# Optimization experiments

Hardware: AMD Instinct MI355X
Metric: run time of the kernel (lower is better)

Reference implementation:

```python
import jax, jax.numpy as jnp
import numpy as np

NUM_HEADS = 16
NEG_INF = -1e18


def setup_inputs() -> dict:
    key = jax.random.key(0)
    ks = jax.random.split(key, 9)
    T, B, D = 2048, 2, 1024
    s = 1.0 / np.sqrt(D)
    return {
        "query": jax.random.normal(ks[0], (T, B, D), jnp.float32),
        "q_w": jax.random.normal(ks[1], (D, D), jnp.float32) * s,
        "q_b": jax.random.normal(ks[2], (D,), jnp.float32) * 0.02,
        "k_w": jax.random.normal(ks[3], (D, D), jnp.float32) * s,
        "k_b": jax.random.normal(ks[4], (D,), jnp.float32) * 0.02,
        "v_w": jax.random.normal(ks[5], (D, D), jnp.float32) * s,
        "v_b": jax.random.normal(ks[6], (D,), jnp.float32) * 0.02,
        "out_w": jax.random.normal(ks[7], (D, D), jnp.float32) * s,
        "out_b": jax.random.normal(ks[8], (D,), jnp.float32) * 0.02,
    }


def reference(query, q_w, q_b, k_w, k_b, v_w, v_b, out_w, out_b):
    # query: [T, B, D] (Time x Batch x Channel). Self-attention, causal mask,
    # dropout=0, need_weights=True.
    T, B, D = query.shape
    H = NUM_HEADS
    hd = D // H
    scaling = 1.0 / jnp.sqrt(jnp.asarray(hd, query.dtype))

    q = (query @ q_w.T + q_b) * scaling
    k = query @ k_w.T + k_b
    v = query @ v_w.T + v_b

    def split_heads(x):  # [T, B, D] -> [B, H, T, hd]
        return x.reshape(T, B, H, hd).transpose(1, 2, 0, 3)

    qh, kh, vh = split_heads(q), split_heads(k), split_heads(v)

    # scores: [B, H, T, T]
    scores = jnp.einsum("bhtd,bhsd->bhts", qh, kh)
    causal = jnp.triu(jnp.full((T, T), NEG_INF, dtype=scores.dtype), k=1)
    scores = scores + causal

    probs = jax.nn.softmax(scores, axis=-1)
    attn = jnp.einsum("bhts,bhsd->bhtd", probs, vh)  # [B, H, T, hd]
    attn = attn.transpose(2, 0, 1, 3).reshape(T, B, D)
    out = attn @ out_w.T + out_b

    # averaged attention weights over heads: [B, T, T]
    avg_weights = probs.sum(axis=1) / H
    return out, avg_weights
```

## Files before the change

kernel.cpp:

```cpp
#include <hip/hip_runtime.h>
#include <hip/hip_bf16.h>
#include <stdint.h>

typedef __hip_bfloat16 bf16;
using short8 = __attribute__((ext_vector_type(8))) short;
using f32x4  = __attribute__((ext_vector_type(4))) float;

#define TDIM 2048
#define BDIM 2
#define DDIM 1024
#define HNUM 16
#define HD   64
#define MDIM 4096
#define M0   16.0f
#define L2E  1.44269504088896f
#define M0B  23.0831207f

__device__ __forceinline__ f32x4 mfma16(short8 a, short8 b, f32x4 c) {
  return __builtin_amdgcn_mfma_f32_16x16x32_bf16(a, b, c, 0, 0, 0);
}

__device__ __forceinline__ float fexp2(float s) {
  return __builtin_amdgcn_exp2f(__builtin_fmaf(s, L2E, -M0B));
}

#define GLD16(G, L)                                              \
  __builtin_amdgcn_global_load_lds(                              \
      (const __attribute__((address_space(1))) void*)(G),        \
      (__attribute__((address_space(3))) void*)(L), 16, 0, 0)

union S8 { short8 v; bf16 h[8]; };
union P4 { uint2 u; bf16 h[4]; };

__global__ __launch_bounds__(256) void cast_all_kernel(
    const float* __restrict__ q, const float* __restrict__ wq,
    const float* __restrict__ wk, const float* __restrict__ wv,
    const float* __restrict__ wo, bf16* __restrict__ dst) {
  int t4 = blockIdx.x * blockDim.x + threadIdx.x;
  int idx = t4 * 4;
  const float* s;
  if (idx < 4194304)      s = q  + idx;
  else if (idx < 5242880) s = wq + (idx - 4194304);
  else if (idx < 6291456) s = wk + (idx - 5242880);
  else if (idx < 7340032) s = wv + (idx - 6291456);
  else                    s = wo + (idx - 7340032);
  float4 v = *(const float4*)s;
  union { ushort4 u; bf16 b[4]; } pk;
  pk.b[0] = __float2bfloat16(v.x);
  pk.b[1] = __float2bfloat16(v.y);
  pk.b[2] = __float2bfloat16(v.z);
  pk.b[3] = __float2bfloat16(v.w);
  *(ushort4*)(dst + idx) = pk.u;
}

__global__ __launch_bounds__(256, 2) void qkv_kernel(
    const bf16* __restrict__ X, const bf16* __restrict__ Wq,
    const bf16* __restrict__ Wk, const bf16* __restrict__ Wv,
    const float* __restrict__ qb, const float* __restrict__ kb,
    const float* __restrict__ vb, bf16* __restrict__ Qo,
    bf16* __restrict__ Ko, bf16* __restrict__ Vto) {
  __shared__ __align__(16) bf16 Xs[128][72];
  __shared__ __align__(16) bf16 Qs[64][72];
  __shared__ __align__(16) bf16 Ks[64][72];
  __shared__ __align__(16) bf16 Vs[64][72];
  const int tid  = threadIdx.x;
  const int lane = tid & 63, wave = tid >> 6;
  const int m0 = blockIdx.y * 128, n0 = blockIdx.x * 64;
  const int wm = (wave >> 1) * 64, wn = (wave & 1) * 32;
  const int fr = lane & 15, quad = lane >> 4, q8 = quad * 8;
  const int r = tid >> 3, cc = (tid & 7) * 8;
  f32x4 aq[4][2] = {}, ak[4][2] = {}, av[2][4] = {};
  const bf16* xp = X  + (size_t)(m0 + r) * DDIM + cc;
  const bf16* qp = Wq + (size_t)(n0 + r) * DDIM + cc;
  const bf16* kp = Wk + (size_t)(n0 + r) * DDIM + cc;
  const bf16* vp = Wv + (size_t)(n0 + r) * DDIM + cc;
  uint4 xv0, xv1, xv2, xv3, qv0, qv1, kv0, kv1, vv0, vv1;
#define QKV_LD(K0)                                                  \
  do {                                                              \
    xv0 = *(const uint4*)(xp + (K0));                               \
    xv1 = *(const uint4*)(xp + (size_t)32 * DDIM + (K0));           \
    xv2 = *(const uint4*)(xp + (size_t)64 * DDIM + (K0));           \
    xv3 = *(const uint4*)(xp + (size_t)96 * DDIM + (K0));           \
    qv0 = *(const uint4*)(qp + (K0));                               \
    qv1 = *(const uint4*)(qp + (size_t)32 * DDIM + (K0));           \
    kv0 = *(const uint4*)(kp + (K0));                               \
    kv1 = *(const uint4*)(kp + (size_t)32 * DDIM + (K0));           \
    vv0 = *(const uint4*)(vp + (K0));                               \
    vv1 = *(const uint4*)(vp + (size_t)32 * DDIM + (K0));           \
  } while (0)
  QKV_LD(0);
  for (int k0 = 0; k0 < DDIM; k0 += 64) {
    __syncthreads();
    *(uint4*)&Xs[r][cc]      = xv0;
    *(uint4*)&Xs[r + 32][cc] = xv1;
    *(uint4*)&Xs[r + 64][cc] = xv2;
    *(uint4*)&Xs[r + 96][cc] = xv3;
    *(uint4*)&Qs[r][cc]      = qv0;
    *(uint4*)&Qs[r + 32][cc] = qv1;
    *(uint4*)&Ks[r][cc]      = kv0;
    *(uint4*)&Ks[r + 32][cc] = kv1;
    *(uint4*)&Vs[r][cc]      = vv0;
    *(uint4*)&Vs[r + 32][cc] = vv1;
    __syncthreads();
    if (k0 + 64 < DDIM) QKV_LD(k0 + 64);
#pragma unroll
    for (int kk = 0; kk < 2; kk++) {
      const int ko = kk * 32 + q8;
      short8 xf[4], qf[2], kf[2], vf[2];
#pragma unroll
      for (int i = 0; i < 4; i++)
        xf[i] = *(const short8*)&Xs[wm + i * 16 + fr][ko];
#pragma unroll
      for (int j = 0; j < 2; j++) {
        qf[j] = *(const short8*)&Qs[wn + j * 16 + fr][ko];
        kf[j] = *(const short8*)&Ks[wn + j * 16 + fr][ko];
        vf[j] = *(const short8*)&Vs[wn + j * 16 + fr][ko];
      }
#pragma unroll
      for (int i = 0; i < 4; i++)
#pragma unroll
        for (int j = 0; j < 2; j++) {
          aq[i][j] = mfma16(xf[i], qf[j], aq[i][j]);
          ak[i][j] = mfma16(xf[i], kf[j], ak[i][j]);
          av[j][i] = mfma16(vf[j], xf[i], av[j][i]);
        }
    }
  }
#undef QKV_LD
#pragma unroll
  for (int mt = 0; mt < 4; mt++)
#pragma unroll
    for (int nt = 0; nt < 2; nt++)
#pragma unroll
      for (int i = 0; i < 4; i++) {
        int gm = m0 + wm + mt * 16 + quad * 4 + i;
        int gn = n0 + wn + nt * 16 + fr;
        int t = gm >> 1, bb = gm & 1, h = gn >> 6, e = gn & 63;
        size_t o = ((size_t)(bb * HNUM + h) * TDIM + t) * HD + e;
        Qo[o] = __float2bfloat16((aq[mt][nt][i] + qb[gn]) * 0.125f);
        Ko[o] = __float2bfloat16(ak[mt][nt][i] + kb[gn]);
      }
#pragma unroll
  for (int vt = 0; vt < 2; vt++)
#pragma unroll
    for (int xt = 0; xt < 4; xt++)
#pragma unroll
      for (int i = 0; i < 4; i++) {
        int gf = n0 + wn + vt * 16 + quad * 4 + i;
        int gt = m0 + wm + xt * 16 + fr;
        int t = gt >> 1, bb = gt & 1, h = gf >> 6, e = gf & 63;
        Vto[((size_t)(bb * HNUM + h) * HD + e) * TDIM + t] =
            __float2bfloat16(av[vt][xt][i] + vb[gf]);
      }
}

__global__ __launch_bounds__(256) void combine_kernel(
    const bf16* __restrict__ P0, const bf16* __restrict__ P1,
    const float* __restrict__ l0buf, const float* __restrict__ l1buf,
    bf16* __restrict__ A) {
  const int idx = (blockIdx.x * 256 + threadIdx.x) * 8;
  const int m = idx >> 10, col = idx & 1023;
  const int t = m >> 1, bb = m & 1, h = col >> 6;
  const size_t li = (size_t)(bb * HNUM + h) * TDIM + t;
  const float inv = 1.0f / (l0buf[li] + l1buf[li]);
  S8 a0, a1, w;
  a0.v = *(const short8*)&P0[idx];
  a1.v = *(const short8*)&P1[idx];
#pragma unroll
  for (int k = 0; k < 8; k++)
    w.h[k] = __float2bfloat16(
        (__bfloat162float(a0.h[k]) + __bfloat162float(a1.h[k])) * inv);
  *(short8*)&A[idx] = w.v;
}

__global__ __launch_bounds__(256) void gemm_out_kernel(
    const bf16* __restrict__ A, const bf16* __restrict__ Bw,
    const float* __restrict__ bias, float* __restrict__ of32) {
  __shared__ __align__(16) bf16 As[64][72];
  __shared__ __align__(16) bf16 Bs[64][72];
  const int tid  = threadIdx.x;
  const int lane = tid & 63, wave = tid >> 6;
  const int m0 = blockIdx.y * 64, n0 = blockIdx.x * 64;
  const int wm = (wave >> 1) * 32, wn = (wave & 1) * 32;
  const int fr = lane & 15, quad = lane >> 4, q8 = quad * 8;
  const int ldr = tid >> 3, ldc = (tid & 7) * 8;
  f32x4 acc[2][2] = {};
  const bf16* ap0 = A + (size_t)(m0 + ldr) * DDIM + ldc;
  const bf16* ap1 = ap0 + (size_t)32 * DDIM;
  const bf16* bp0 = Bw + (size_t)(n0 + ldr) * DDIM + ldc;
  const bf16* bp1 = bp0 + (size_t)32 * DDIM;
  uint4 av0, av1, bv0, bv1;
#define OUT_LD(K0)                                  \
  do {                                              \
    av0 = *(const uint4*)(ap0 + (K0));              \
    av1 = *(const uint4*)(ap1 + (K0));              \
    bv0 = *(const uint4*)(bp0 + (K0));              \
    bv1 = *(const uint4*)(bp1 + (K0));              \
  } while (0)
  OUT_LD(0);
  for (int k0 = 0; k0 < DDIM; k0 += 64) {
    __syncthreads();
    *(uint4*)&As[ldr][ldc]      = av0;
    *(uint4*)&As[ldr + 32][ldc] = av1;
    *(uint4*)&Bs[ldr][ldc]      = bv0;
    *(uint4*)&Bs[ldr + 32][ldc] = bv1;
    __syncthreads();
    if (k0 + 64 < DDIM) OUT_LD(k0 + 64);
#pragma unroll
    for (int kk = 0; kk < 2; kk++) {
      const int ko = kk * 32 + q8;
      short8 af0, af1, bf0, bf1;
      af0 = *(const short8*)&As[wm + fr][ko];
      af1 = *(const short8*)&As[wm + 16 + fr][ko];
      bf0 = *(const short8*)&Bs[wn + fr][ko];
      bf1 = *(const short8*)&Bs[wn + 16 + fr][ko];
      acc[0][0] = mfma16(af0, bf0, acc[0][0]);
      acc[0][1] = mfma16(af0, bf1, acc[0][1]);
      acc[1][0] = mfma16(af1, bf0, acc[1][0]);
      acc[1][1] = mfma16(af1, bf1, acc[1][1]);
    }
  }
#undef OUT_LD
#pragma unroll
  for (int mt = 0; mt < 2; mt++)
#pragma unroll
    for (int nt = 0; nt < 2; nt++)
#pragma unroll
      for (int i = 0; i < 4; i++) {
        int gm = m0 + wm + mt * 16 + quad * 4 + i;
        int gn = n0 + wn + nt * 16 + fr;
        of32[(size_t)gm * DDIM + gn] = acc[mt][nt][i] + bias[gn];
      }
}

__global__ __launch_bounds__(256) void attn_split_kernel(
    const bf16* __restrict__ Q, const bf16* __restrict__ K,
    const bf16* __restrict__ Vt, bf16* __restrict__ P0o,
    bf16* __restrict__ P1o, float* __restrict__ l0buf,
    float* __restrict__ l1buf) {
  __shared__ __align__(16) bf16 Ks[2][64][40];
  __shared__ __align__(16) bf16 Vs[2][64][40];
  __shared__ __align__(16) bf16 pt[4][32][72];
  const int tid = threadIdx.x, lane = tid & 63, wave = tid >> 6;
  const int bid = blockIdx.x;
  const int part = bid & 1, bh = (bid >> 1) & 31, t128 = 15 - (bid >> 6);
  const int b = bh >> 4, h = bh & 15;
  const int t0 = t128 * 128 + wave * 32;
  const int fr = lane & 15, quad = lane >> 4, q8 = quad * 8;
  const bf16* Qp = Q + ((size_t)bh * TDIM + t0) * HD;
  const bf16* Kp = K + (size_t)bh * TDIM * HD;
  const bf16* Vp = Vt + (size_t)bh * HD * TDIM;
  short8 aq[2][2];
  aq[0][0] = *(const short8*)&Qp[fr * HD + q8];
  aq[0][1] = *(const short8*)&Qp[fr * HD + 32 + q8];
  aq[1][0] = *(const short8*)&Qp[(16 + fr) * HD + q8];
  aq[1][1] = *(const short8*)&Qp[(16 + fr) * HD + 32 + q8];
  const int Cb = 2 * t128 + 2, C0 = t128 + 1;
  const int clo = part ? C0 : 0, chi = part ? Cb : C0;
  const int sr0 = tid >> 3, scc = (tid & 7) * 8, sr1 = sr0 + 32;
  const int ssub = scc >> 5, scol = scc & 31;
  f32x4 oacc[2][4] = {};
  float lsum[2] = {0.f, 0.f};
  uint4 kv0, kv1, vv0, vv1;
  auto ldglob = [&](int c) {
    int s0 = c * 64;
    kv0 = *(const uint4*)&Kp[(size_t)(s0 + sr0) * HD + scc];
    kv1 = *(const uint4*)&Kp[(size_t)(s0 + sr1) * HD + scc];
    vv0 = *(const uint4*)&Vp[(size_t)sr0 * TDIM + s0 + scc];
    vv1 = *(const uint4*)&Vp[(size_t)sr1 * TDIM + s0 + scc];
  };
  ldglob(clo);
  for (int c = clo; c < chi; c++) {
    __syncthreads();
    *(uint4*)&Ks[ssub][sr0][scol] = kv0;
    *(uint4*)&Ks[ssub][sr1][scol] = kv1;
    *(uint4*)&Vs[ssub][sr0][scol] = vv0;
    *(uint4*)&Vs[ssub][sr1][scol] = vv1;
    __syncthreads();
    if (c + 1 < chi) ldglob(c + 1);
    const int s0 = c * 64;
    if (s0 > t0 + 31) continue;
    f32x4 scT[2][4] = {};
#pragma unroll
    for (int j = 0; j < 4; j++) {
      short8 k0f = *(const short8*)&Ks[0][j * 16 + fr][q8];
      short8 k1f = *(const short8*)&Ks[1][j * 16 + fr][q8];
      scT[0][j] = mfma16(k0f, aq[0][0], scT[0][j]);
      scT[0][j] = mfma16(k1f, aq[0][1], scT[0][j]);
      scT[1][j] = mfma16(k0f, aq[1][0], scT[1][j]);
      scT[1][j] = mfma16(k1f, aq[1][1], scT[1][j]);
    }
#pragma unroll
    for (int g = 0; g < 2; g++) {
      const int tg = t0 + g * 16;
#pragma unroll
      for (int j = 0; j < 4; j++) {
        const int sj = s0 + j * 16;
        P4 pk;
        if (sj > tg + 15) {
          pk.u = make_uint2(0u, 0u);
        } else if (sj + 15 <= tg) {
#pragma unroll
          for (int i = 0; i < 4; i++) {
            float p = fexp2(scT[g][j][i]);
            lsum[g] += p;
            pk.h[i] = __float2bfloat16(p);
          }
        } else {
          const int t_row = tg + fr;
          const int s_base = sj + quad * 4;
#pragma unroll
          for (int i = 0; i < 4; i++) {
            float p = 0.f;
            if (s_base + i <= t_row) {
              p = fexp2(scT[g][j][i]);
              lsum[g] += p;
            }
            pk.h[i] = __float2bfloat16(p);
          }
        }
        *(uint2*)&pt[wave][g * 16 + fr][j * 16 + quad * 4] = pk.u;
      }
    }
#pragma unroll
    for (int c2 = 0; c2 < 2; c2++) {
      short8 ap0 = *(const short8*)&pt[wave][fr][c2 * 32 + q8];
      short8 ap1 = *(const short8*)&pt[wave][16 + fr][c2 * 32 + q8];
#pragma unroll
      for (int nt = 0; nt < 4; nt++) {
        short8 vf = *(const short8*)&Vs[c2][nt * 16 + fr][q8];
        oacc[0][nt] = mfma16(ap0, vf, oacc[0][nt]);
        oacc[1][nt] = mfma16(ap1, vf, oacc[1][nt]);
      }
    }
  }
  float lr[2];
#pragma unroll
  for (int g = 0; g < 2; g++) {
    float l = lsum[g];
    l += __shfl_xor(l, 16);
    l += __shfl_xor(l, 32);
    lr[g] = l;
  }
  bf16*  Op = part ? P1o : P0o;
  float* lb = part ? l1buf : l0buf;
#pragma unroll
  for (int g = 0; g < 2; g++)
#pragma unroll
    for (int nt = 0; nt < 4; nt++)
#pragma unroll
      for (int i = 0; i < 4; i++) {
        int t_row = t0 + g * 16 + quad * 4 + i;
        int col = h * HD + nt * 16 + fr;
        Op[((size_t)t_row * BDIM + b) * DDIM + col] =
            __float2bfloat16(oacc[g][nt][i]);
      }
  if (quad == 0) {
    lb[(size_t)bh * TDIM + t0 + fr]      = lr[0];
    lb[(size_t)bh * TDIM + t0 + 16 + fr] = lr[1];
  }
}

__global__ __launch_bounds__(256) void avg_kernel(
    const bf16* __restrict__ Q, const bf16* __restrict__ K,
    const float* __restrict__ l0buf, const float* __restrict__ l1buf,
    float* __restrict__ avgw) {
  const int tid = threadIdx.x;
  int r = blockIdx.x;
  const int b = (r >= 2048) ? 1 : 0;
  r &= 2047;
  float* avp = avgw + (size_t)b * TDIM * TDIM;
  if (r >= 1056) {
    int r2 = r - 1056;
    int ti = 0;
    while (ti < 31 && (ti + 1) * (62 - ti) <= r2) ti++;
    int si = (2 * ti + 2) + (r2 - ti * (63 - ti));
    int t0b = ti * 64, s0 = si * 32;
#pragma unroll
    for (int k = 0; k < 2; k++) {
      int off = (tid * 2 + k) * 4;
      *(float4*)&avp[(size_t)(t0b + (off >> 5)) * TDIM + s0 + (off & 31)] =
          make_float4(0.f, 0.f, 0.f, 0.f);
    }
    return;
  }
  int ti = 0;
  while ((ti + 1) * (ti + 2) <= r) ti++;
  const int si = r - ti * (ti + 1);
  const int t0b = ti * 64, s0 = si * 32;

  __shared__ __align__(16) bf16 Qs[2][64][64];
  __shared__ __align__(16) bf16 Ks2[2][32][64];
  __shared__ float sinvl[HNUM][64];
#pragma unroll
  for (int k = 0; k < 4; k++) {
    int idx = tid + k * 256;
    size_t li = (size_t)(b * HNUM + (idx >> 6)) * TDIM + t0b + (idx & 63);
    sinvl[idx >> 6][idx & 63] = 1.0f / (l0buf[li] + l1buf[li]);
  }
  const int lane = tid & 63, wave = tid >> 6;
  const int fr = lane & 15, quad = lane >> 4;
  const int twr = wave * 16, tw = t0b + twr;
  const int srow8 = lane >> 3;
  const int scol = (((lane & 7) ^ (srow8 & 7))) * 8;
  const bf16* Qb = Q + (size_t)b * HNUM * TDIM * HD;
  const bf16* Kb = K + (size_t)b * HNUM * TDIM * HD;
#define AVG_STAGE(B, HH)                                                      \
  do {                                                                        \
    const bf16* Qh_ = Qb + (size_t)(HH) * TDIM * HD;                          \
    const bf16* Kh_ = Kb + (size_t)(HH) * TDIM * HD;                          \
    GLD16(Qh_ + (size_t)(t0b + 16 * wave + srow8) * HD + scol,                \
          &Qs[B][16 * wave][0]);                                              \
    GLD16(Qh_ + (size_t)(t0b + 16 * wave + 8 + srow8) * HD + scol,            \
          &Qs[B][16 * wave + 8][0]);                                          \
    GLD16(Kh_ + (size_t)(s0 + 8 * wave + srow8) * HD + scol,                  \
          &Ks2[B][8 * wave][0]);                                              \
  } while (0)
  AVG_STAGE(0, 0);
  const int sA0 = ((quad)     ^ (fr & 7)) * 8;
  const int sA1 = ((4 + quad) ^ (fr & 7)) * 8;
  f32x4 facc[2] = {};
  const bool d0 = (s0 > tw + 15),      f0 = (s0 + 15 <= tw);
  const bool d1 = (s0 + 16 > tw + 15), f1 = (s0 + 31 <= tw);
  for (int hh = 0; hh < HNUM; hh++) {
    const int cur = hh & 1;
    __syncthreads();
    if (hh + 1 < HNUM) AVG_STAGE(cur ^ 1, hh + 1);
    f32x4 sv = *(const f32x4*)&sinvl[hh][twr + quad * 4];
    short8 a0 = *(const short8*)&Qs[cur][twr + fr][sA0];
    short8 a1 = *(const short8*)&Qs[cur][twr + fr][sA1];
    if (!d0) {
      short8 b0 = *(const short8*)&Ks2[cur][fr][sA0];
      short8 b1 = *(const short8*)&Ks2[cur][fr][sA1];
      f32x4 sc = {};
      sc = mfma16(a0, b0, sc);
      sc = mfma16(a1, b1, sc);
      if (f0) {
#pragma unroll
        for (int i = 0; i < 4; i++)
          facc[0][i] += fexp2(sc[i]) * sv[i];
      } else {
#pragma unroll
        for (int i = 0; i < 4; i++)
          if (s0 + fr <= tw + quad * 4 + i)
            facc[0][i] += fexp2(sc[i]) * sv[i];
      }
    }
    if (!d1) {
      short8 b0 = *(const short8*)&Ks2[cur][16 + fr][sA0];
      short8 b1 = *(const short8*)&Ks2[cur][16 + fr][sA1];
      f32x4 sc = {};
      sc = mfma16(a0, b0, sc);
      sc = mfma16(a1, b1, sc);
      if (f1) {
#pragma unroll
        for (int i = 0; i < 4; i++)
          facc[1][i] += fexp2(sc[i]) * sv[i];
      } else {
#pragma unroll
        for (int i = 0; i < 4; i++)
          if (s0 + 16 + fr <= tw + quad * 4 + i)
            facc[1][i] += fexp2(sc[i]) * sv[i];
      }
    }
  }
#undef AVG_STAGE
#pragma unroll
  for (int nt = 0; nt < 2; nt++)
#pragma unroll
    for (int i = 0; i < 4; i++)
      avp[(size_t)(t0b + twr + quad * 4 + i) * TDIM + s0 + nt * 16 + fr] =
          facc[nt][i] * 0.0625f;
}

extern "C" void kernel_launch(void* const* d_in, const int* in_sizes, int n_in,
                              void* d_out, int out_size, void* d_ws, size_t ws_size,
                              hipStream_t stream) {
  const float* q   = (const float*)d_in[0];
  const float* q_w = (const float*)d_in[1];
  const float* q_b = (const float*)d_in[2];
  const float* k_w = (const float*)d_in[3];
  const float* k_b = (const float*)d_in[4];
  const float* v_w = (const float*)d_in[5];
  const float* v_b = (const float*)d_in[6];
  const float* o_w = (const float*)d_in[7];
  const float* o_b = (const float*)d_in[8];
  float* out = (float*)d_out;
  float* avg = out + (size_t)MDIM * DDIM;

  bf16* ws  = (bf16*)d_ws;
  bf16* Xbf = ws;
  bf16* Wq  = ws + 4194304;
  bf16* Wk  = ws + 5242880;
  bf16* Wv  = ws + 6291456;
  bf16* Wo  = ws + 7340032;
  bf16* Qw  = ws + 8388608;
  bf16* Kw  = ws + 12582912;
  bf16* Vt  = ws + 16777216;
  bf16* P1  = ws + 20971520;
  bf16* P0  = ws;
  bf16* Ab  = ws + 16777216;
  float* l0 = (float*)(ws + 4194304);
  float* l1 = (float*)(ws + 4325376);

  cast_all_kernel<<<8192, 256, 0, stream>>>(q, q_w, k_w, v_w, o_w, Xbf);
  qkv_kernel<<<dim3(16, 32), 256, 0, stream>>>(Xbf, Wq, Wk, Wv, q_b, k_b, v_b,
                                               Qw, Kw, Vt);
  attn_split_kernel<<<1024, 256, 0, stream>>>(Qw, Kw, Vt, P0, P1, l0, l1);
  combine_kernel<<<2048, 256, 0, stream>>>(P0, P1, l0, l1, Ab);
  avg_kernel<<<4096, 256, 0, stream>>>(Qw, Kw, l0, l1, avg);
  gemm_out_kernel<<<dim3(16, 64), 256, 0, stream>>>(Ab, Wo, o_b, out);
}
```

Before: 222.1 us.

## Enlarge output GEMM and head-averaged weight tiles for more reuse

The output projection GEMM now computes 128x64 tiles per block, with each wave owning a 64x32 sub-tile, which halves the grid and reuses B-fragments across more MFMAs. The avg_kernel now processes 64x64 causal score tiles instead of 64x32, so each Q tile staged per head serves twice as many keys. Its block indexing is reworked for the new triangular enumeration, while the zero-fill blocks stay in 32-column units. Larger tiles mean more registers and LDS per block and fewer blocks, which may reduce occupancy and load balance.

Result: slower. 228.0 us (+2.6%).

```diff
diff --git a/kernel.cpp b/kernel.cpp
--- a/kernel.cpp
+++ b/kernel.cpp
@@ -173,56 +173,61 @@
   *(short8*)&A[idx] = w.v;
 }
 
-__global__ __launch_bounds__(256) void gemm_out_kernel(
+__global__ __launch_bounds__(256, 2) void gemm_out_kernel(
     const bf16* __restrict__ A, const bf16* __restrict__ Bw,
     const float* __restrict__ bias, float* __restrict__ of32) {
-  __shared__ __align__(16) bf16 As[64][72];
+  __shared__ __align__(16) bf16 As[128][72];
   __shared__ __align__(16) bf16 Bs[64][72];
   const int tid  = threadIdx.x;
   const int lane = tid & 63, wave = tid >> 6;
-  const int m0 = blockIdx.y * 64, n0 = blockIdx.x * 64;
-  const int wm = (wave >> 1) * 32, wn = (wave & 1) * 32;
+  const int m0 = blockIdx.y * 128, n0 = blockIdx.x * 64;
+  const int wm = (wave >> 1) * 64, wn = (wave & 1) * 32;
   const int fr = lane & 15, quad = lane >> 4, q8 = quad * 8;
-  const int ldr = tid >> 3, ldc = (tid & 7) * 8;
-  f32x4 acc[2][2] = {};
-  const bf16* ap0 = A + (size_t)(m0 + ldr) * DDIM + ldc;
-  const bf16* ap1 = ap0 + (size_t)32 * DDIM;
-  const bf16* bp0 = Bw + (size_t)(n0 + ldr) * DDIM + ldc;
-  const bf16* bp1 = bp0 + (size_t)32 * DDIM;
-  uint4 av0, av1, bv0, bv1;
-#define OUT_LD(K0)                                  \
-  do {                                              \
-    av0 = *(const uint4*)(ap0 + (K0));              \
-    av1 = *(const uint4*)(ap1 + (K0));              \
-    bv0 = *(const uint4*)(bp0 + (K0));              \
-    bv1 = *(const uint4*)(bp1 + (K0));              \
+  const int r = tid >> 3, cc = (tid & 7) * 8;
+  f32x4 acc[4][2] = {};
+  const bf16* ap = A  + (size_t)(m0 + r) * DDIM + cc;
+  const bf16* bp = Bw + (size_t)(n0 + r) * DDIM + cc;
+  uint4 av0, av1, av2, av3, bv0, bv1;
+#define OUT_LD(K0)                                                  \
+  do {                                                              \
+    av0 = *(const uint4*)(ap + (K0));                               \
+    av1 = *(const uint4*)(ap + (size_t)32 * DDIM + (K0));           \
+    av2 = *(const uint4*)(ap + (size_t)64 * DDIM + (K0));           \
+    av3 = *(const uint4*)(ap + (size_t)96 * DDIM + (K0));           \
+    bv0 = *(const uint4*)(bp + (K0));                               \
+    bv1 = *(const uint4*)(bp + (size_t)32 * DDIM + (K0));           \
   } while (0)
   OUT_LD(0);
   for (int k0 = 0; k0 < DDIM; k0 += 64) {
     __syncthreads();
-    *(uint4*)&As[ldr][ldc]      = av0;
-    *(uint4*)&As[ldr + 32][ldc] = av1;
-    *(uint4*)&Bs[ldr][ldc]      = bv0;
-    *(uint4*)&Bs[ldr + 32][ldc] = bv1;
+    *(uint4*)&As[r][cc]      = av0;
+    *(uint4*)&As[r + 32][cc] = av1;
+    *(uint4*)&As[r + 64][cc] = av2;
+    *(uint4*)&As[r + 96][cc] = av3;
+    *(uint4*)&Bs[r][cc]      = bv0;
+    *(uint4*)&Bs[r + 32][cc] = bv1;
     __syncthreads();
     if (k0 + 64 < DDIM) OUT_LD(k0 + 64);
 #pragma unroll
     for (int kk = 0; kk < 2; kk++) {
       const int ko = kk * 32 + q8;
-      short8 af0, af1, bf0, bf1;
-      af0 = *(const short8*)&As[wm + fr][ko];
-      af1 = *(const short8*)&As[wm + 16 + fr][ko];
-      bf0 = *(const short8*)&Bs[wn + fr][ko];
-      bf1 = *(const short8*)&Bs[wn + 16 + fr][ko];
-      acc[0][0] = mfma16(af0, bf0, acc[0][0]);
-      acc[0][1] = mfma16(af0, bf1, acc[0][1]);
-      acc[1][0] = mfma16(af1, bf0, acc[1][0]);
-      acc[1][1] = mfma16(af1, bf1, acc[1][1]);
+      short8 af[4], bfr[2];
+#pragma unroll
+      for (int i = 0; i < 4; i++)
+        af[i] = *(const short8*)&As[wm + i * 16 + fr][ko];
+#pragma unroll
+      for (int j = 0; j < 2; j++)
+        bfr[j] = *(const short8*)&Bs[wn + j * 16 + fr][ko];
+#pragma unroll
+      for (int i = 0; i < 4; i++)
+#pragma unroll
+        for (int j = 0; j < 2; j++)
+          acc[i][j] = mfma16(af[i], bfr[j], acc[i][j]);
     }
   }
 #undef OUT_LD
 #pragma unroll
-  for (int mt = 0; mt < 2; mt++)
+  for (int mt = 0; mt < 4; mt++)
 #pragma unroll
     for (int nt = 0; nt < 2; nt++)
 #pragma unroll
@@ -367,11 +372,11 @@
     float* __restrict__ avgw) {
   const int tid = threadIdx.x;
   int r = blockIdx.x;
-  const int b = (r >= 2048) ? 1 : 0;
-  r &= 2047;
+  const int b = (r >= 1520) ? 1 : 0;
+  if (b) r -= 1520;
   float* avp = avgw + (size_t)b * TDIM * TDIM;
-  if (r >= 1056) {
-    int r2 = r - 1056;
+  if (r >= 528) {
+    int r2 = r - 528;
     int ti = 0;
     while (ti < 31 && (ti + 1) * (62 - ti) <= r2) ti++;
     int si = (2 * ti + 2) + (r2 - ti * (63 - ti));
@@ -385,12 +390,12 @@
     return;
   }
   int ti = 0;
-  while ((ti + 1) * (ti + 2) <= r) ti++;
-  const int si = r - ti * (ti + 1);
-  const int t0b = ti * 64, s0 = si * 32;
+  while ((ti + 1) * (ti + 2) / 2 <= r) ti++;
+  const int kp = r - ti * (ti + 1) / 2;
+  const int t0b = ti * 64, sA = kp * 64;
 
   __shared__ __align__(16) bf16 Qs[2][64][64];
-  __shared__ __align__(16) bf16 Ks2[2][32][64];
+  __shared__ __align__(16) bf16 Ks[2][64][64];
   __shared__ float sinvl[HNUM][64];
 #pragma unroll
   for (int k = 0; k < 4; k++) {
@@ -402,7 +407,7 @@
   const int fr = lane & 15, quad = lane >> 4;
   const int twr = wave * 16, tw = t0b + twr;
   const int srow8 = lane >> 3;
-  const int scol = (((lane & 7) ^ (srow8 & 7))) * 8;
+  const int scol = ((lane & 7) ^ (srow8 & 7)) * 8;
   const bf16* Qb = Q + (size_t)b * HNUM * TDIM * HD;
   const bf16* Kb = K + (size_t)b * HNUM * TDIM * HD;
 #define AVG_STAGE(B, HH)                                                      \
@@ -413,64 +418,60 @@
           &Qs[B][16 * wave][0]);                                              \
     GLD16(Qh_ + (size_t)(t0b + 16 * wave + 8 + srow8) * HD + scol,            \
           &Qs[B][16 * wave + 8][0]);                                          \
-    GLD16(Kh_ + (size_t)(s0 + 8 * wave + srow8) * HD + scol,                  \
-          &Ks2[B][8 * wave][0]);                                              \
+    GLD16(Kh_ + (size_t)(sA + 16 * wave + srow8) * HD + scol,                 \
+          &Ks[B][16 * wave][0]);                                              \
+    GLD16(Kh_ + (size_t)(sA + 16 * wave + 8 + srow8) * HD + scol,             \
+          &Ks[B][16 * wave + 8][0]);                                          \
   } while (0)
   AVG_STAGE(0, 0);
-  const int sA0 = ((quad)     ^ (fr & 7)) * 8;
-  const int sA1 = ((4 + quad) ^ (fr & 7)) * 8;
-  f32x4 facc[2] = {};
-  const bool d0 = (s0 > tw + 15),      f0 = (s0 + 15 <= tw);
-  const bool d1 = (s0 + 16 > tw + 15), f1 = (s0 + 31 <= tw);
+  const int sl0 = ((quad)     ^ (fr & 7)) * 8;
+  const int sl1 = ((4 + quad) ^ (fr & 7)) * 8;
+  f32x4 facc[2][2] = {};
+  const bool dd00 = (sA      > tw + 15), ff00 = (sA + 15 <= tw);
+  const bool dd01 = (sA + 16 > tw + 15), ff01 = (sA + 31 <= tw);
+  const bool dd10 = (sA + 32 > tw + 15), ff10 = (sA + 47 <= tw);
+  const bool dd11 = (sA + 48 > tw + 15), ff11 = (sA + 63 <= tw);
   for (int hh = 0; hh < HNUM; hh++) {
     const int cur = hh & 1;
     __syncthreads();
     if (hh + 1 < HNUM) AVG_STAGE(cur ^ 1, hh + 1);
     f32x4 sv = *(const f32x4*)&sinvl[hh][twr + quad * 4];
-    short8 a0 = *(const short8*)&Qs[cur][twr + fr][sA0];
-    short8 a1 = *(const short8*)&Qs[cur][twr + fr][sA1];
-    if (!d0) {
-      short8 b0 = *(const short8*)&Ks2[cur][fr][sA0];
-      short8 b1 = *(const short8*)&Ks2[cur][fr][sA1];
-      f32x4 sc = {};
-      sc = mfma16(a0, b0, sc);
-      sc = mfma16(a1, b1, sc);
-      if (f0) {
-#pragma unroll
-        for (int i = 0; i < 4; i++)
-          facc[0][i] += fexp2(sc[i]) * sv[i];
-      } else {
-#pragma unroll
-        for (int i = 0; i < 4; i++)
-          if (s0 + fr <= tw + quad * 4 + i)
-            facc[0][i] += fexp2(sc[i]) * sv[i];
-      }
-    }
-    if (!d1) {
-      short8 b0 = *(const short8*)&Ks2[cur][16 + fr][sA0];
-      short8 b1 = *(const short8*)&Ks2[cur][16 + fr][sA1];
-      f32x4 sc = {};
-      sc = mfma16(a0, b0, sc);
-      sc = mfma16(a1, b1, sc);
-      if (f1) {
-#pragma unroll
-        for (int i = 0; i < 4; i++)
-          facc[1][i] += fexp2(sc[i]) * sv[i];
-      } else {
-#pragma unroll
-        for (int i = 0; i < 4; i++)
-          if (s0 + 16 + fr <= tw + quad * 4 + i)
-            facc[1][i] += fexp2(sc[i]) * sv[i];
-      }
-    }
+    short8 a0 = *(const short8*)&Qs[cur][twr + fr][sl0];
+    short8 a1 = *(const short8*)&Qs[cur][twr + fr][sl1];
+#define AVG_SUB(T, NT, DEAD, FULL)                                            \
+    if (!(DEAD)) {                                                            \
+      const int krow = (T) * 32 + (NT) * 16 + fr;                             \
+      short8 b0 = *(const short8*)&Ks[cur][krow][sl0];                        \
+      short8 b1 = *(const short8*)&Ks[cur][krow][sl1];                        \
+      f32x4 sc = {};                                                          \
+      sc = mfma16(a0, b0, sc);                                                \
+      sc = mfma16(a1, b1, sc);                                                \
+      if (FULL) {                                                             \
+        _Pragma("unroll")                                                     \
+        for (int i = 0; i < 4; i++)                                           \
+          facc[T][NT][i] += fexp2(sc[i]) * sv[i];                             \
+      } else {                                                                \
+        _Pragma("unroll")                                                     \
+        for (int i = 0; i < 4; i++)                                           \
+          if (sA + (T) * 32 + (NT) * 16 + fr <= tw + quad * 4 + i)            \
+            facc[T][NT][i] += fexp2(sc[i]) * sv[i];                           \
+      }                                                                       \
+    }
+    AVG_SUB(0, 0, dd00, ff00)
+    AVG_SUB(0, 1, dd01, ff01)
+    AVG_SUB(1, 0, dd10, ff10)
+    AVG_SUB(1, 1, dd11, ff11)
+#undef AVG_SUB
   }
 #undef AVG_STAGE
 #pragma unroll
-  for (int nt = 0; nt < 2; nt++)
-#pragma unroll
-    for (int i = 0; i < 4; i++)
-      avp[(size_t)(t0b + twr + quad * 4 + i) * TDIM + s0 + nt * 16 + fr] =
-          facc[nt][i] * 0.0625f;
+  for (int T = 0; T < 2; T++)
+#pragma unroll
+    for (int nt = 0; nt < 2; nt++)
+#pragma unroll
+      for (int i = 0; i < 4; i++)
+        avp[(size_t)(tw + quad * 4 + i) * TDIM + sA + T * 32 + nt * 16 + fr] =
+            facc[T][nt][i] * 0.0625f;
 }
 
 extern "C" void kernel_launch(void* const* d_in, const int* in_sizes, int n_in,
@@ -508,6 +509,6 @@
                                                Qw, Kw, Vt);
   attn_split_kernel<<<1024, 256, 0, stream>>>(Qw, Kw, Vt, P0, P1, l0, l1);
   combine_kernel<<<2048, 256, 0, stream>>>(P0, P1, l0, l1, Ab);
-  avg_kernel<<<4096, 256, 0, stream>>>(Qw, Kw, l0, l1, avg);
-  gemm_out_kernel<<<dim3(16, 64), 256, 0, stream>>>(Ab, Wo, o_b, out);
-}
+  avg_kernel<<<3040, 256, 0, stream>>>(Qw, Kw, l0, l1, avg);
+  gemm_out_kernel<<<dim3(16, 32), 256, 0, stream>>>(Ab, Wo, o_b, out);
+}
```

## Enlarge avg-weights tiles to 128x64 and keep Q fragments in registers

Applied to the files above, without the earlier changes.

The averaged-attention-weights kernel now has each block cover a 128x64 tile instead of 64x32, with each wave handling 32 query rows against 64 key columns. Q fragments are loaded straight from global memory into registers and double-buffered across heads, while only K goes through shared memory. Together this cuts the block count by four, reuses each K tile across more rows and drops the Q staging in LDS. The cost is more registers per thread, coarser causal granularity so more masked work per tile, and fewer blocks to fill the GPU.

New measurement: 223.9 us. About the same (+0.8%).

```diff
diff --git a/kernel.cpp b/kernel.cpp
--- a/kernel.cpp
+++ b/kernel.cpp
@@ -366,111 +366,125 @@
     const float* __restrict__ l0buf, const float* __restrict__ l1buf,
     float* __restrict__ avgw) {
   const int tid = threadIdx.x;
-  int r = blockIdx.x;
-  const int b = (r >= 2048) ? 1 : 0;
-  r &= 2047;
+  int gid = blockIdx.x;
+  if (gid >= 544) {
+    int z = gid - 544;
+    const int b = (z >= 240) ? 1 : 0;
+    if (b) z -= 240;
+    int ti1 = 0;
+    while (ti1 < 15 && (30 * (ti1 + 1) - (ti1 + 1) * ti1) <= z) ti1++;
+    int si = (2 * ti1 + 2) + (z - (30 * ti1 - ti1 * (ti1 - 1)));
+    int t0b = ti1 * 128, s0 = si * 64;
+    float* avp = avgw + (size_t)b * TDIM * TDIM;
+#pragma unroll
+    for (int k = 0; k < 8; k++) {
+      int e = (tid + k * 256) * 4;
+      *(float4*)&avp[(size_t)(t0b + (e >> 6)) * TDIM + s0 + (e & 63)] =
+          make_float4(0.f, 0.f, 0.f, 0.f);
+    }
+    return;
+  }
+  const int b = (gid >= 272) ? 1 : 0;
+  int r = gid - (b ? 272 : 0);
+  int ti1 = 0;
+  while (ti1 < 15 && (ti1 + 1) * (ti1 + 2) <= r) ti1++;
+  const int si = r - ti1 * (ti1 + 1);
+  const int t0b = ti1 * 128, s0 = si * 64;
   float* avp = avgw + (size_t)b * TDIM * TDIM;
-  if (r >= 1056) {
-    int r2 = r - 1056;
-    int ti = 0;
-    while (ti < 31 && (ti + 1) * (62 - ti) <= r2) ti++;
-    int si = (2 * ti + 2) + (r2 - ti * (63 - ti));
-    int t0b = ti * 64, s0 = si * 32;
-#pragma unroll
-    for (int k = 0; k < 2; k++) {
-      int off = (tid * 2 + k) * 4;
-      *(float4*)&avp[(size_t)(t0b + (off >> 5)) * TDIM + s0 + (off & 31)] =
-          make_float4(0.f, 0.f, 0.f, 0.f);
-    }
-    return;
-  }
-  int ti = 0;
-  while ((ti + 1) * (ti + 2) <= r) ti++;
-  const int si = r - ti * (ti + 1);
-  const int t0b = ti * 64, s0 = si * 32;
-
-  __shared__ __align__(16) bf16 Qs[2][64][64];
-  __shared__ __align__(16) bf16 Ks2[2][32][64];
-  __shared__ float sinvl[HNUM][64];
-#pragma unroll
-  for (int k = 0; k < 4; k++) {
+
+  __shared__ __align__(16) bf16 Ks[2][64][64];
+  __shared__ float sinvl[HNUM][128];
+#pragma unroll
+  for (int k = 0; k < 8; k++) {
     int idx = tid + k * 256;
-    size_t li = (size_t)(b * HNUM + (idx >> 6)) * TDIM + t0b + (idx & 63);
-    sinvl[idx >> 6][idx & 63] = 1.0f / (l0buf[li] + l1buf[li]);
+    size_t li = (size_t)(b * HNUM + (idx >> 7)) * TDIM + t0b + (idx & 127);
+    sinvl[idx >> 7][idx & 127] = 1.0f / (l0buf[li] + l1buf[li]);
   }
   const int lane = tid & 63, wave = tid >> 6;
-  const int fr = lane & 15, quad = lane >> 4;
-  const int twr = wave * 16, tw = t0b + twr;
+  const int fr = lane & 15, quad = lane >> 4, q8 = quad * 8;
+  const int tw = t0b + wave * 32;
+  const bool wlive = (s0 <= tw + 31);
   const int srow8 = lane >> 3;
-  const int scol = (((lane & 7) ^ (srow8 & 7))) * 8;
+  const int scol = ((lane & 7) ^ (srow8 & 7)) * 8;
+  const int sl0 = ((quad)     ^ (fr & 7)) * 8;
+  const int sl1 = ((4 + quad) ^ (fr & 7)) * 8;
   const bf16* Qb = Q + (size_t)b * HNUM * TDIM * HD;
   const bf16* Kb = K + (size_t)b * HNUM * TDIM * HD;
-#define AVG_STAGE(B, HH)                                                      \
-  do {                                                                        \
-    const bf16* Qh_ = Qb + (size_t)(HH) * TDIM * HD;                          \
-    const bf16* Kh_ = Kb + (size_t)(HH) * TDIM * HD;                          \
-    GLD16(Qh_ + (size_t)(t0b + 16 * wave + srow8) * HD + scol,                \
-          &Qs[B][16 * wave][0]);                                              \
-    GLD16(Qh_ + (size_t)(t0b + 16 * wave + 8 + srow8) * HD + scol,            \
-          &Qs[B][16 * wave + 8][0]);                                          \
-    GLD16(Kh_ + (size_t)(s0 + 8 * wave + srow8) * HD + scol,                  \
-          &Ks2[B][8 * wave][0]);                                              \
+#define AVG_STAGEK(B, HH)                                               \
+  do {                                                                  \
+    const bf16* Kh_ = Kb + (size_t)(HH) * TDIM * HD;                    \
+    GLD16(Kh_ + (size_t)(s0 + 16 * wave + srow8) * HD + scol,           \
+          &Ks[B][16 * wave][0]);                                        \
+    GLD16(Kh_ + (size_t)(s0 + 16 * wave + 8 + srow8) * HD + scol,       \
+          &Ks[B][16 * wave + 8][0]);                                    \
   } while (0)
-  AVG_STAGE(0, 0);
-  const int sA0 = ((quad)     ^ (fr & 7)) * 8;
-  const int sA1 = ((4 + quad) ^ (fr & 7)) * 8;
-  f32x4 facc[2] = {};
-  const bool d0 = (s0 > tw + 15),      f0 = (s0 + 15 <= tw);
-  const bool d1 = (s0 + 16 > tw + 15), f1 = (s0 + 31 <= tw);
+#define AVG_LOADQ(P, HH)                                                   \
+  do {                                                                    \
+    const bf16* Qh_ = Qb + (size_t)(HH) * TDIM * HD;                      \
+    P[0][0] = *(const short8*)&Qh_[(size_t)(tw + fr) * HD + q8];          \
+    P[0][1] = *(const short8*)&Qh_[(size_t)(tw + fr) * HD + 32 + q8];     \
+    P[1][0] = *(const short8*)&Qh_[(size_t)(tw + 16 + fr) * HD + q8];     \
+    P[1][1] = *(const short8*)&Qh_[(size_t)(tw + 16 + fr) * HD + 32 + q8];\
+  } while (0)
+  bool dead[2][4], full[2][4];
+#pragma unroll
+  for (int ts = 0; ts < 2; ts++)
+#pragma unroll
+    for (int cg = 0; cg < 4; cg++) {
+      dead[ts][cg] = (s0 + cg * 16 > tw + ts * 16 + 15);
+      full[ts][cg] = (s0 + cg * 16 + 15 <= tw + ts * 16);
+    }
+  short8 qf[2][2][2];
+  AVG_STAGEK(0, 0);
+  if (wlive) AVG_LOADQ(qf[0], 0);
+  f32x4 facc[2][4] = {};
+#pragma unroll
   for (int hh = 0; hh < HNUM; hh++) {
     const int cur = hh & 1;
     __syncthreads();
-    if (hh + 1 < HNUM) AVG_STAGE(cur ^ 1, hh + 1);
-    f32x4 sv = *(const f32x4*)&sinvl[hh][twr + quad * 4];
-    short8 a0 = *(const short8*)&Qs[cur][twr + fr][sA0];
-    short8 a1 = *(const short8*)&Qs[cur][twr + fr][sA1];
-    if (!d0) {
-      short8 b0 = *(const short8*)&Ks2[cur][fr][sA0];
-      short8 b1 = *(const short8*)&Ks2[cur][fr][sA1];
-      f32x4 sc = {};
-      sc = mfma16(a0, b0, sc);
-      sc = mfma16(a1, b1, sc);
-      if (f0) {
-#pragma unroll
-        for (int i = 0; i < 4; i++)
-          facc[0][i] += fexp2(sc[i]) * sv[i];
-      } else {
-#pragma unroll
-        for (int i = 0; i < 4; i++)
-          if (s0 + fr <= tw + quad * 4 + i)
-            facc[0][i] += fexp2(sc[i]) * sv[i];
-      }
-    }
-    if (!d1) {
-      short8 b0 = *(const short8*)&Ks2[cur][16 + fr][sA0];
-      short8 b1 = *(const short8*)&Ks2[cur][16 + fr][sA1];
-      f32x4 sc = {};
-      sc = mfma16(a0, b0, sc);
-      sc = mfma16(a1, b1, sc);
-      if (f1) {
-#pragma unroll
-        for (int i = 0; i < 4; i++)
-          facc[1][i] += fexp2(sc[i]) * sv[i];
-      } else {
-#pragma unroll
-        for (int i = 0; i < 4; i++)
-          if (s0 + 16 + fr <= tw + quad * 4 + i)
-            facc[1][i] += fexp2(sc[i]) * sv[i];
-      }
-    }
-  }
-#undef AVG_STAGE
-#pragma unroll
-  for (int nt = 0; nt < 2; nt++)
-#pragma unroll
-    for (int i = 0; i < 4; i++)
-      avp[(size_t)(t0b + twr + quad * 4 + i) * TDIM + s0 + nt * 16 + fr] =
-          facc[nt][i] * 0.0625f;
+    if (hh + 1 < HNUM) {
+      AVG_STAGEK(cur ^ 1, hh + 1);
+      if (wlive) AVG_LOADQ(qf[cur ^ 1], hh + 1);
+    }
+    if (!wlive) continue;
+    short8 kb[4][2];
+#pragma unroll
+    for (int cg = 0; cg < 4; cg++) {
+      kb[cg][0] = *(const short8*)&Ks[cur][cg * 16 + fr][sl0];
+      kb[cg][1] = *(const short8*)&Ks[cur][cg * 16 + fr][sl1];
+    }
+#pragma unroll
+    for (int ts = 0; ts < 2; ts++) {
+      f32x4 sv = *(const f32x4*)&sinvl[hh][32 * wave + ts * 16 + quad * 4];
+#pragma unroll
+      for (int cg = 0; cg < 4; cg++) {
+        if (dead[ts][cg]) continue;
+        f32x4 sc = {};
+        sc = mfma16(qf[cur][ts][0], kb[cg][0], sc);
+        sc = mfma16(qf[cur][ts][1], kb[cg][1], sc);
+        if (full[ts][cg]) {
+#pragma unroll
+          for (int i = 0; i < 4; i++)
+            facc[ts][cg][i] += fexp2(sc[i]) * sv[i];
+        } else {
+#pragma unroll
+          for (int i = 0; i < 4; i++)
+            if (s0 + cg * 16 + fr <= tw + ts * 16 + quad * 4 + i)
+              facc[ts][cg][i] += fexp2(sc[i]) * sv[i];
+        }
+      }
+    }
+  }
+#undef AVG_STAGEK
+#undef AVG_LOADQ
+#pragma unroll
+  for (int ts = 0; ts < 2; ts++)
+#pragma unroll
+    for (int cg = 0; cg < 4; cg++)
+#pragma unroll
+      for (int i = 0; i < 4; i++)
+        avp[(size_t)(tw + ts * 16 + quad * 4 + i) * TDIM + s0 + cg * 16 + fr] =
+            facc[ts][cg][i] * 0.0625f;
 }
 
 extern "C" void kernel_launch(void* const* d_in, const int* in_sizes, int n_in,
@@ -508,6 +522,6 @@
                                                Qw, Kw, Vt);
   attn_split_kernel<<<1024, 256, 0, stream>>>(Qw, Kw, Vt, P0, P1, l0, l1);
   combine_kernel<<<2048, 256, 0, stream>>>(P0, P1, l0, l1, Ab);
-  avg_kernel<<<4096, 256, 0, stream>>>(Qw, Kw, l0, l1, avg);
+  avg_kernel<<<1024, 256, 0, stream>>>(Qw, Kw, l0, l1, avg);
   gemm_out_kernel<<<dim3(16, 64), 256, 0, stream>>>(Ab, Wo, o_b, out);
 }
```
